# Optimization experiments

Hardware: AMD Instinct MI355X
Metric: run time of the kernel (lower is better)

The kernel has to match this reference:

```python
import jax, jax.numpy as jnp
import numpy as np

K = 2  # top-k experts per token

def setup_inputs() -> dict:
    key = jax.random.key(0)
    ks = jax.random.split(key, 8)
    B, S, D, F, E = 2, 1024, 1024, 4096, 8
    s_in = 1.0 / np.sqrt(D)
    s_mid = 1.0 / np.sqrt(F)
    return {
        "x": jax.random.normal(ks[0], (B, S, D), dtype=jnp.float32),
        "Wr": jax.random.uniform(ks[1], (D, E), jnp.float32, -s_in, s_in),
        "br": jax.random.uniform(ks[2], (E,), jnp.float32, -s_in, s_in),
        "W1": jax.random.uniform(ks[3], (E, D, F), jnp.float32, -s_in, s_in),
        "b1": jax.random.uniform(ks[4], (E, F), jnp.float32, -s_in, s_in),
        "W2": jax.random.uniform(ks[5], (E, F, D), jnp.float32, -s_mid, s_mid),
        "b2": jax.random.uniform(ks[6], (E, D), jnp.float32, -s_mid, s_mid),
    }

def _moe(x, Wr, br, W1, b1, W2, b2):
    E = Wr.shape[1]
    # router (eval mode: no noise)
    logits = jnp.einsum('bsd,de->bse', x, Wr) + br          # [B,S,E]
    topk_logits, topk_idx = jax.lax.top_k(logits, K)        # [B,S,K]
    router_probs = jax.nn.softmax(topk_logits, axis=-1)     # [B,S,K]
    # per-expert combine weight: sum over k slots assigned to expert e
    onehot = jax.nn.one_hot(topk_idx, E, dtype=x.dtype)     # [B,S,K,E]
    w = jnp.einsum('bske,bsk->bse', onehot, router_probs)   # [B,S,E]
    # scan over experts (fixed small E), accumulate weighted expert outputs
    def step(acc, ew):
        W1j, b1j, W2j, b2j, wj = ew                          # wj: [B,S]
        h = jax.nn.gelu(jnp.einsum('bsd,df->bsf', x, W1j) + b1j, approximate=False)
        y = jnp.einsum('bsf,fd->bsd', h, W2j) + b2j
        return acc + y * wj[..., None], None
    out, _ = jax.lax.scan(step, jnp.zeros_like(x),
                          (W1, b1, W2, b2, jnp.transpose(w, (2, 0, 1))))
    return out, router_probs

def reference(x, Wr, br, W1, b1, W2, b2):
    return _moe(x, Wr, br, W1, b1, W2, b2)
```

## Files before the change

kernel.cpp:

```cpp
#include <hip/hip_runtime.h>
#include <hip/hip_bf16.h>
#include <cstdint>

#define TOKENS 2048
#define Dm 1024
#define Fm 4096
#define Em 8

typedef short s16x8 __attribute__((ext_vector_type(8)));
typedef float f32x4 __attribute__((ext_vector_type(4)));

#define GLOAD16(g, l) __builtin_amdgcn_global_load_lds(                     \
    (const __attribute__((address_space(1))) void*)(g),                     \
    (__attribute__((address_space(3))) void*)(l), 16, 0, 0)

__device__ __forceinline__ ushort f2bf(float f) {
  union { float f; uint32_t u; } v; v.f = f;
  uint32_t r = v.u + 0x7fffu + ((v.u >> 16) & 1u);
  return (ushort)(r >> 16);
}

__device__ __forceinline__ void kstep(const ushort* sbuf, int eoff, int aidx,
                                      int bidx, f32x4 (&acc)[4][4]) {
  s16x8 av[4], bv[4];
#pragma unroll
  for (int m = 0; m < 4; ++m)
    av[m] = *(const s16x8*)(sbuf + eoff + aidx + m * 512);
#pragma unroll
  for (int n = 0; n < 4; ++n)
    bv[n] = *(const s16x8*)(sbuf + eoff + 4096 + bidx + n * 512);
#pragma unroll
  for (int m = 0; m < 4; ++m)
#pragma unroll
    for (int n = 0; n < 4; ++n)
      acc[m][n] = __builtin_amdgcn_mfma_f32_16x16x32_bf16(av[m], bv[n], acc[m][n], 0, 0, 0);
}

#define STAGE4(boff) {                                                      \
    char* bb = (char*)sbuf + (boff);                                        \
    GLOAD16(sA0, bb + wid * 1024);                                          \
    GLOAD16(sA1, bb + 4096 + wid * 1024);                                   \
    GLOAD16(sB0, bb + 8192 + wid * 1024);                                   \
    GLOAD16(sB1, bb + 12288 + wid * 1024);                                  \
    sA0 += 32; sA1 += 32; sB0 += 32; sB1 += 32; }

__global__ void transcvt(const float* __restrict__ in, ushort* __restrict__ out,
                         int R, int C) {
  __shared__ float tile[32 * 33];
  int e = blockIdx.z;
  const float* src = in + (size_t)e * R * C;
  ushort* dst = out + (size_t)e * R * C;
  int c0 = blockIdx.x * 32, r0 = blockIdx.y * 32;
  int lr = threadIdx.x >> 5, lc = threadIdx.x & 31;
#pragma unroll
  for (int p = 0; p < 4; ++p)
    tile[(p * 8 + lr) * 33 + lc] = src[(size_t)(r0 + p * 8 + lr) * C + c0 + lc];
  __syncthreads();
#pragma unroll
  for (int p = 0; p < 4; ++p)
    dst[(size_t)(c0 + p * 8 + lr) * R + r0 + lc] = f2bf(tile[lc * 33 + p * 8 + lr]);
}

__global__ void prep(const float* __restrict__ W1, ushort* __restrict__ W1T,
                     const float* __restrict__ W2, ushort* __restrict__ W2T,
                     int do_w2,
                     const float* __restrict__ x, const float* __restrict__ Wr,
                     const float* __restrict__ br, float* __restrict__ probs,
                     int* __restrict__ e_sel, float* __restrict__ w_sel,
                     ushort* __restrict__ xb) {
  __shared__ float shf[32 * 33];
  int b = blockIdx.x;
  if (b < 65536) {
    const float* src;
    ushort* dst;
    size_t sstride, dstride;
    if (b < 32768) {
      int cx = b & 127, ry = (b >> 7) & 31, e = b >> 12;
      src = W1 + ((size_t)e * Dm + ry * 32) * Fm + cx * 32;
      dst = W1T + ((size_t)e * Fm + cx * 32) * Dm + ry * 32;
      sstride = Fm; dstride = Dm;
    } else {
      if (!do_w2) return;
      int b2i = b - 32768;
      int cx = b2i & 31, ry = (b2i >> 5) & 127, e = b2i >> 12;
      src = W2 + ((size_t)e * Fm + ry * 32) * Dm + cx * 32;
      dst = W2T + ((size_t)e * Dm + cx * 32) * Fm + ry * 32;
      sstride = Dm; dstride = Fm;
    }
    int lr = threadIdx.x >> 5, lc = threadIdx.x & 31;
#pragma unroll
    for (int p = 0; p < 4; ++p)
      shf[(p * 8 + lr) * 33 + lc] = src[(size_t)(p * 8 + lr) * sstride + lc];
    __syncthreads();
#pragma unroll
    for (int p = 0; p < 4; ++p)
      dst[(size_t)(p * 8 + lr) * dstride + lc] = f2bf(shf[lc * 33 + p * 8 + lr]);
    return;
  }
  int t = b - 65536;
  const float4* xr4 = (const float4*)(x + (size_t)t * Dm);
  float4 v = xr4[threadIdx.x];
  ushort4 o;
  o.x = f2bf(v.x); o.y = f2bf(v.y); o.z = f2bf(v.z); o.w = f2bf(v.w);
  ((ushort4*)(xb + (size_t)t * Dm))[threadIdx.x] = o;

  int d0 = threadIdx.x * 4;
  const float4* wr4 = (const float4*)(Wr + (size_t)d0 * Em);
  float wv[4][8];
#pragma unroll
  for (int r = 0; r < 4; ++r) {
    float4 a = wr4[r * 2], bq = wr4[r * 2 + 1];
    wv[r][0] = a.x; wv[r][1] = a.y; wv[r][2] = a.z; wv[r][3] = a.w;
    wv[r][4] = bq.x; wv[r][5] = bq.y; wv[r][6] = bq.z; wv[r][7] = bq.w;
  }
  float xs[4] = {v.x, v.y, v.z, v.w};
  float acc[Em];
#pragma unroll
  for (int e = 0; e < Em; ++e)
    acc[e] = xs[0] * wv[0][e] + xs[1] * wv[1][e] + xs[2] * wv[2][e] + xs[3] * wv[3][e];
#pragma unroll
  for (int off = 32; off >= 1; off >>= 1)
#pragma unroll
    for (int e = 0; e < Em; ++e) acc[e] += __shfl_down(acc[e], off);
  float* red = shf;
  int lane = threadIdx.x & 63, wid = threadIdx.x >> 6;
  if (lane == 0)
#pragma unroll
    for (int e = 0; e < Em; ++e) red[wid * 8 + e] = acc[e];
  __syncthreads();
  if (threadIdx.x == 0) {
    float lg[Em];
#pragma unroll
    for (int e = 0; e < Em; ++e)
      lg[e] = red[e] + red[8 + e] + red[16 + e] + red[24 + e] + br[e];
    int i0 = 0;
    for (int e = 1; e < Em; ++e) if (lg[e] > lg[i0]) i0 = e;
    int i1 = -1;
    for (int e = 0; e < Em; ++e) {
      if (e == i0) continue;
      if (i1 < 0 || lg[e] > lg[i1]) i1 = e;
    }
    float d = lg[i1] - lg[i0];
    float tt = expf(d);
    float inv = 1.f / (1.f + tt);
    probs[t * 2] = inv; probs[t * 2 + 1] = tt * inv;
    e_sel[t * 2] = i0; e_sel[t * 2 + 1] = i1;
    w_sel[t * 2] = inv; w_sel[t * 2 + 1] = tt * inv;
  }
}

__global__ void build_lists(const int* __restrict__ e_sel, const float* __restrict__ w_sel,
                            int* __restrict__ tok_of_row, float* __restrict__ w_of_row,
                            int* __restrict__ base, int* __restrict__ npad) {
  __shared__ int cnt[Em], run[Em], sbase[Em];
  __shared__ int wsum[4][Em];
  int tid = threadIdx.x, lane = tid & 63, wid = tid >> 6;
  if (tid < Em) { cnt[tid] = 0; run[tid] = 0; }
  __syncthreads();
  for (int t = tid; t < TOKENS; t += 256) {
    atomicAdd(&cnt[e_sel[2 * t]], 1);
    atomicAdd(&cnt[e_sel[2 * t + 1]], 1);
  }
  __syncthreads();
  if (tid == 0) {
    int b = 0;
    for (int e = 0; e < Em; ++e) {
      base[e] = b; sbase[e] = b;
      int n = cnt[e];
      int p = (n + 127) & ~127;
      npad[e] = p; b += p;
    }
  }
  __syncthreads();
  for (int c = 0; c < TOKENS / 256; ++c) {
    int t = c * 256 + tid;
    int e0 = e_sel[2 * t], e1 = e_sel[2 * t + 1];
    unsigned long long mm[Em];
#pragma unroll
    for (int e = 0; e < Em; ++e) {
      unsigned long long m0 = __ballot(e0 == e);
      unsigned long long m1 = __ballot(e1 == e);
      mm[e] = m0 | m1;
      if (lane == 0) wsum[wid][e] = __popcll(mm[e]);
    }
    __syncthreads();
    unsigned long long below = (1ull << lane) - 1ull;
    {
      int e = e0;
      int p = __popcll(mm[e] & below);
      int pre = 0;
      for (int w = 0; w < wid; ++w) pre += wsum[w][e];
      int row = sbase[e] + run[e] + pre + p;
      tok_of_row[row] = t; w_of_row[row] = w_sel[2 * t];
    }
    {
      int e = e1;
      int p = __popcll(mm[e] & below);
      int pre = 0;
      for (int w = 0; w < wid; ++w) pre += wsum[w][e];
      int row = sbase[e] + run[e] + pre + p;
      tok_of_row[row] = t; w_of_row[row] = w_sel[2 * t + 1];
    }
    __syncthreads();
    if (tid < Em) {
      int s = 0;
      for (int w = 0; w < 4; ++w) s += wsum[w][tid];
      run[tid] += s;
    }
    __syncthreads();
  }
  for (int e = 0; e < Em; ++e) {
    int n = cnt[e];
    int p = (n + 127) & ~127;
    for (int i = n + tid; i < p; i += 256) {
      tok_of_row[sbase[e] + i] = -1;
      w_of_row[sbase[e] + i] = 0.f;
    }
  }
}

__global__ __launch_bounds__(256) void gemm1(
    const ushort* __restrict__ xb, const ushort* __restrict__ W1T,
    const float* __restrict__ b1, ushort* __restrict__ H,
    const int* __restrict__ tok_of_row, const int* __restrict__ base,
    const int* __restrict__ npad) {
  __shared__ ushort sbuf[16384];
  __shared__ int toks[128];
  int tid = threadIdx.x, lane = tid & 63, wid = tid >> 6;
  int e = blockIdx.y >> 4, rt = blockIdx.y & 15;
  int nt = npad[e] >> 7;
  if (rt >= nt) return;
  int row0 = base[e] + rt * 128;
  int n0 = blockIdx.x * 128;
  if (tid < 128) toks[tid] = tok_of_row[row0 + tid];
  __syncthreads();
  int arow = tid >> 2, asub = tid & 3;
  int sw = ((asub ^ ((arow >> 1) & 3)) << 3);
  int t0 = toks[arow];      if (t0 < 0) t0 = 0;
  int t1 = toks[64 + arow]; if (t1 < 0) t1 = 0;
  const ushort* sA0 = xb + (size_t)t0 * Dm + sw;
  const ushort* sA1 = xb + (size_t)t1 * Dm + sw;
  const ushort* sB0 = W1T + ((size_t)e * Fm + n0 + arow) * Dm + sw;
  const ushort* sB1 = sB0 + (size_t)64 * Dm;
  int wr2 = wid >> 1, wc2 = wid & 1;
  int g = lane >> 4, c = (lane >> 1) & 3;
  int aidx = (wr2 * 64 + (lane & 15)) * 32 + ((g ^ c) << 3);
  int bidx = (wc2 * 64 + (lane & 15)) * 32 + ((g ^ c) << 3);
  f32x4 acc[4][4] = {};
  STAGE4(0)
  __syncthreads();
  for (int t = 0; t < 30; t += 2) {
    STAGE4(16384)
    kstep(sbuf, 0, aidx, bidx, acc);
    __syncthreads();
    STAGE4(0)
    kstep(sbuf, 8192, aidx, bidx, acc);
    __syncthreads();
  }
  STAGE4(16384)
  kstep(sbuf, 0, aidx, bidx, acc);
  __syncthreads();
  kstep(sbuf, 8192, aidx, bidx, acc);
#pragma unroll
  for (int p = 0; p < 2; ++p) {
    if (wr2 == p) {
#pragma unroll
      for (int n = 0; n < 4; ++n) {
        int col = wc2 * 64 + (lane & 15) + n * 16;
        float bias = b1[e * Fm + n0 + col];
#pragma unroll
        for (int m = 0; m < 4; ++m) {
#pragma unroll
          for (int j = 0; j < 4; ++j) {
            float v = acc[m][n][j] + bias;
            float gl = 0.5f * v * (1.f + erff(v * 0.70710678118654752f));
            sbuf[(g * 4 + m * 16 + j) * 128 + col] = f2bf(gl);
          }
        }
      }
    }
    __syncthreads();
#pragma unroll
    for (int q = 0; q < 4; ++q) {
      int id = q * 256 + tid;
      int r = id >> 4, ch = id & 15;
      *(s16x8*)(H + (size_t)(row0 + p * 64 + r) * Fm + n0 + ch * 8) =
          *(const s16x8*)(sbuf + r * 128 + ch * 8);
    }
    __syncthreads();
  }
}

__global__ __launch_bounds__(256) void gemm2(
    const ushort* __restrict__ H, const ushort* __restrict__ W2T,
    const float* __restrict__ b2,
    const int* __restrict__ tok_of_row, const float* __restrict__ w_of_row,
    const int* __restrict__ base, const int* __restrict__ npad,
    float* __restrict__ out) {
  __shared__ ushort sbuf[16384];
  __shared__ int toks[128];
  __shared__ float wts[128];
  int tid = threadIdx.x, lane = tid & 63, wid = tid >> 6;
  int e = blockIdx.y >> 4, rt = blockIdx.y & 15;
  int nt = npad[e] >> 7;
  if (rt >= nt) return;
  int row0 = base[e] + rt * 128;
  int n0 = blockIdx.x * 128;
  int k0 = blockIdx.z * (Fm / 2);
  if (tid < 128) {
    toks[tid] = tok_of_row[row0 + tid];
    wts[tid] = w_of_row[row0 + tid];
  }
  __syncthreads();
  int arow = tid >> 2, asub = tid & 3;
  int sw = ((asub ^ ((arow >> 1) & 3)) << 3);
  const ushort* sA0 = H + (size_t)(row0 + arow) * Fm + k0 + sw;
  const ushort* sA1 = sA0 + (size_t)64 * Fm;
  const ushort* sB0 = W2T + ((size_t)e * Dm + n0 + arow) * Fm + k0 + sw;
  const ushort* sB1 = sB0 + (size_t)64 * Fm;
  int wr2 = wid >> 1, wc2 = wid & 1;
  int g = lane >> 4, c = (lane >> 1) & 3;
  int aidx = (wr2 * 64 + (lane & 15)) * 32 + ((g ^ c) << 3);
  int bidx = (wc2 * 64 + (lane & 15)) * 32 + ((g ^ c) << 3);
  f32x4 acc[4][4] = {};
  STAGE4(0)
  __syncthreads();
  for (int t = 0; t < 62; t += 2) {
    STAGE4(16384)
    kstep(sbuf, 0, aidx, bidx, acc);
    __syncthreads();
    STAGE4(0)
    kstep(sbuf, 8192, aidx, bidx, acc);
    __syncthreads();
  }
  STAGE4(16384)
  kstep(sbuf, 0, aidx, bidx, acc);
  __syncthreads();
  kstep(sbuf, 8192, aidx, bidx, acc);
  int rb = wr2 * 64 + g * 4;
  int cb = n0 + wc2 * 64 + (lane & 15);
  int add_bias = (blockIdx.z == 0);
#pragma unroll
  for (int n = 0; n < 4; ++n) {
    int col = cb + n * 16;
    float bias = add_bias ? b2[e * Dm + col] : 0.f;
#pragma unroll
    for (int m = 0; m < 4; ++m) {
      int rl = rb + m * 16;
#pragma unroll
      for (int j = 0; j < 4; ++j) {
        int tok = toks[rl + j];
        if (tok >= 0)
          atomicAdd(&out[(size_t)tok * Dm + col], wts[rl + j] * (acc[m][n][j] + bias));
      }
    }
  }
}

extern "C" void kernel_launch(void* const* d_in, const int* in_sizes, int n_in,
                              void* d_out, int out_size, void* d_ws, size_t ws_size,
                              hipStream_t stream) {
  const float* x  = (const float*)d_in[0];
  const float* Wr = (const float*)d_in[1];
  const float* br = (const float*)d_in[2];
  const float* W1 = (const float*)d_in[3];
  const float* b1 = (const float*)d_in[4];
  const float* W2 = (const float*)d_in[5];
  const float* b2 = (const float*)d_in[6];
  float* out = (float*)d_out;
  float* probs = out + (size_t)TOKENS * Dm;

  char* ws = (char*)d_ws;
  ushort* W1T  = (ushort*)ws;
  ushort* Hbuf = (ushort*)(ws + 67108864);
  ushort* xb   = (ushort*)(ws + 109051904);
  int*   tok_of_row = (int*)(ws + 113246208);
  float* w_of_row   = (float*)(ws + 113266688);
  int*   e_sel      = (int*)(ws + 113287168);
  float* w_sel      = (float*)(ws + 113303552);
  int*   meta       = (int*)(ws + 113319936);
  int sep = (ws_size >= 180429056ULL) ? 1 : 0;
  ushort* W2T = sep ? (ushort*)(ws + 113320192) : W1T;

  hipMemsetAsync(out, 0, (size_t)TOKENS * Dm * sizeof(float), stream);
  prep<<<65536 + TOKENS, 256, 0, stream>>>(W1, W1T, W2, W2T, sep, x, Wr, br,
                                           probs, e_sel, w_sel, xb);
  build_lists<<<1, 256, 0, stream>>>(e_sel, w_sel, tok_of_row, w_of_row,
                                     meta, meta + 8);
  gemm1<<<dim3(32, 128), 256, 0, stream>>>(xb, W1T, b1, Hbuf, tok_of_row,
                                           meta, meta + 8);
  if (!sep)
    transcvt<<<dim3(Dm / 32, Fm / 32, Em), 256, 0, stream>>>(W2, W2T, Fm, Dm);
  gemm2<<<dim3(8, 128, 2), 256, 0, stream>>>(Hbuf, W2T, b2, tok_of_row, w_of_row,
                                             meta, meta + 8, out);
}
```

Measured before the change: 325.9 us.

## Widen weight-transpose tiles, deepen GEMM prefetch pipeline, split gemm2 K four ways

The weight-conversion transpose now handles 64x64 tiles with float4 loads and ushort4 stores, replacing 32x32 scalar accesses and cutting the block count. Both GEMMs now prefetch two stages ahead and use explicit vmcnt/lgkmcnt waits with raw barriers in place of __syncthreads, so global-to-LDS loads can overlap the MFMA work. gemm2 splits K four ways instead of two, which gives more blocks but doubles the atomicAdd traffic into the output. The hand-written waitcnt counts and the LDS reuse after the epilogue must match the load issue order exactly, or the results will be wrong.

Measured after the change: 343.8 us. 5.5% more time.

```diff
diff --git a/kernel.cpp b/kernel.cpp
--- a/kernel.cpp
+++ b/kernel.cpp
@@ -13,6 +13,12 @@
 #define GLOAD16(g, l) __builtin_amdgcn_global_load_lds(                     \
     (const __attribute__((address_space(1))) void*)(g),                     \
     (__attribute__((address_space(3))) void*)(l), 16, 0, 0)
+
+#define VM4 asm volatile("s_waitcnt vmcnt(4)" ::: "memory")
+#define VM0 asm volatile("s_waitcnt vmcnt(0)" ::: "memory")
+#define LG0 asm volatile("s_waitcnt lgkmcnt(0)" ::: "memory")
+#define SCH __builtin_amdgcn_sched_barrier(0)
+#define BAR do { SCH; __builtin_amdgcn_s_barrier(); SCH; } while (0)
 
 __device__ __forceinline__ ushort f2bf(float f) {
   union { float f; uint32_t u; } v; v.f = f;
@@ -68,43 +74,56 @@
                      const float* __restrict__ br, float* __restrict__ probs,
                      int* __restrict__ e_sel, float* __restrict__ w_sel,
                      ushort* __restrict__ xb) {
-  __shared__ float shf[32 * 33];
+  __shared__ float tile[64 * 65];
   int b = blockIdx.x;
-  if (b < 65536) {
+  int tid = threadIdx.x;
+  if (b < 16384) {
     const float* src;
     ushort* dst;
     size_t sstride, dstride;
-    if (b < 32768) {
-      int cx = b & 127, ry = (b >> 7) & 31, e = b >> 12;
-      src = W1 + ((size_t)e * Dm + ry * 32) * Fm + cx * 32;
-      dst = W1T + ((size_t)e * Fm + cx * 32) * Dm + ry * 32;
+    if (b < 8192) {
+      int cx = b & 63, ry = (b >> 6) & 15, e = b >> 10;
+      src = W1 + ((size_t)e * Dm + ry * 64) * Fm + cx * 64;
+      dst = W1T + ((size_t)e * Fm + cx * 64) * Dm + ry * 64;
       sstride = Fm; dstride = Dm;
     } else {
       if (!do_w2) return;
-      int b2i = b - 32768;
-      int cx = b2i & 31, ry = (b2i >> 5) & 127, e = b2i >> 12;
-      src = W2 + ((size_t)e * Fm + ry * 32) * Dm + cx * 32;
-      dst = W2T + ((size_t)e * Dm + cx * 32) * Fm + ry * 32;
+      int j = b - 8192;
+      int cx = j & 15, ry = (j >> 4) & 63, e = j >> 10;
+      src = W2 + ((size_t)e * Fm + ry * 64) * Dm + cx * 64;
+      dst = W2T + ((size_t)e * Dm + cx * 64) * Fm + ry * 64;
       sstride = Dm; dstride = Fm;
     }
-    int lr = threadIdx.x >> 5, lc = threadIdx.x & 31;
-#pragma unroll
-    for (int p = 0; p < 4; ++p)
-      shf[(p * 8 + lr) * 33 + lc] = src[(size_t)(p * 8 + lr) * sstride + lc];
-    __syncthreads();
-#pragma unroll
-    for (int p = 0; p < 4; ++p)
-      dst[(size_t)(p * 8 + lr) * dstride + lc] = f2bf(shf[lc * 33 + p * 8 + lr]);
+    int lr = tid >> 4, lc4 = (tid & 15) * 4;
+#pragma unroll
+    for (int p = 0; p < 4; ++p) {
+      float4 v = *(const float4*)(src + (size_t)(p * 16 + lr) * sstride + lc4);
+      tile[(p * 16 + lr) * 65 + lc4] = v.x;
+      tile[(p * 16 + lr) * 65 + lc4 + 1] = v.y;
+      tile[(p * 16 + lr) * 65 + lc4 + 2] = v.z;
+      tile[(p * 16 + lr) * 65 + lc4 + 3] = v.w;
+    }
+    __syncthreads();
+#pragma unroll
+    for (int p = 0; p < 4; ++p) {
+      int oc = p * 16 + lr;
+      ushort4 o;
+      o.x = f2bf(tile[(lc4 + 0) * 65 + oc]);
+      o.y = f2bf(tile[(lc4 + 1) * 65 + oc]);
+      o.z = f2bf(tile[(lc4 + 2) * 65 + oc]);
+      o.w = f2bf(tile[(lc4 + 3) * 65 + oc]);
+      *(ushort4*)(dst + (size_t)oc * dstride + lc4) = o;
+    }
     return;
   }
-  int t = b - 65536;
+  int t = b - 16384;
   const float4* xr4 = (const float4*)(x + (size_t)t * Dm);
-  float4 v = xr4[threadIdx.x];
+  float4 v = xr4[tid];
   ushort4 o;
   o.x = f2bf(v.x); o.y = f2bf(v.y); o.z = f2bf(v.z); o.w = f2bf(v.w);
-  ((ushort4*)(xb + (size_t)t * Dm))[threadIdx.x] = o;
-
-  int d0 = threadIdx.x * 4;
+  ((ushort4*)(xb + (size_t)t * Dm))[tid] = o;
+
+  int d0 = tid * 4;
   const float4* wr4 = (const float4*)(Wr + (size_t)d0 * Em);
   float wv[4][8];
 #pragma unroll
@@ -122,13 +141,13 @@
   for (int off = 32; off >= 1; off >>= 1)
 #pragma unroll
     for (int e = 0; e < Em; ++e) acc[e] += __shfl_down(acc[e], off);
-  float* red = shf;
-  int lane = threadIdx.x & 63, wid = threadIdx.x >> 6;
+  float* red = tile;
+  int lane = tid & 63, wid = tid >> 6;
   if (lane == 0)
 #pragma unroll
     for (int e = 0; e < Em; ++e) red[wid * 8 + e] = acc[e];
   __syncthreads();
-  if (threadIdx.x == 0) {
+  if (tid == 0) {
     float lg[Em];
 #pragma unroll
     for (int e = 0; e < Em; ++e)
@@ -248,18 +267,20 @@
   int bidx = (wc2 * 64 + (lane & 15)) * 32 + ((g ^ c) << 3);
   f32x4 acc[4][4] = {};
   STAGE4(0)
-  __syncthreads();
+  STAGE4(16384)
   for (int t = 0; t < 30; t += 2) {
+    VM4; BAR;
+    kstep(sbuf, 0, aidx, bidx, acc);
+    LG0; BAR;
+    STAGE4(0)
+    VM4; BAR;
+    kstep(sbuf, 8192, aidx, bidx, acc);
+    LG0; BAR;
     STAGE4(16384)
-    kstep(sbuf, 0, aidx, bidx, acc);
-    __syncthreads();
-    STAGE4(0)
-    kstep(sbuf, 8192, aidx, bidx, acc);
-    __syncthreads();
-  }
-  STAGE4(16384)
+  }
+  VM4; BAR;
   kstep(sbuf, 0, aidx, bidx, acc);
-  __syncthreads();
+  LG0; VM0; BAR;
   kstep(sbuf, 8192, aidx, bidx, acc);
 #pragma unroll
   for (int p = 0; p < 2; ++p) {
@@ -306,7 +327,7 @@
   if (rt >= nt) return;
   int row0 = base[e] + rt * 128;
   int n0 = blockIdx.x * 128;
-  int k0 = blockIdx.z * (Fm / 2);
+  int k0 = blockIdx.z * (Fm / 4);
   if (tid < 128) {
     toks[tid] = tok_of_row[row0 + tid];
     wts[tid] = w_of_row[row0 + tid];
@@ -324,18 +345,20 @@
   int bidx = (wc2 * 64 + (lane & 15)) * 32 + ((g ^ c) << 3);
   f32x4 acc[4][4] = {};
   STAGE4(0)
-  __syncthreads();
-  for (int t = 0; t < 62; t += 2) {
+  STAGE4(16384)
+  for (int t = 0; t < 30; t += 2) {
+    VM4; BAR;
+    kstep(sbuf, 0, aidx, bidx, acc);
+    LG0; BAR;
+    STAGE4(0)
+    VM4; BAR;
+    kstep(sbuf, 8192, aidx, bidx, acc);
+    LG0; BAR;
     STAGE4(16384)
-    kstep(sbuf, 0, aidx, bidx, acc);
-    __syncthreads();
-    STAGE4(0)
-    kstep(sbuf, 8192, aidx, bidx, acc);
-    __syncthreads();
-  }
-  STAGE4(16384)
+  }
+  VM4; BAR;
   kstep(sbuf, 0, aidx, bidx, acc);
-  __syncthreads();
+  LG0; VM0; BAR;
   kstep(sbuf, 8192, aidx, bidx, acc);
   int rb = wr2 * 64 + g * 4;
   int cb = n0 + wc2 * 64 + (lane & 15);
@@ -383,7 +406,7 @@
   ushort* W2T = sep ? (ushort*)(ws + 113320192) : W1T;
 
   hipMemsetAsync(out, 0, (size_t)TOKENS * Dm * sizeof(float), stream);
-  prep<<<65536 + TOKENS, 256, 0, stream>>>(W1, W1T, W2, W2T, sep, x, Wr, br,
+  prep<<<16384 + TOKENS, 256, 0, stream>>>(W1, W1T, W2, W2T, sep, x, Wr, br,
                                            probs, e_sel, w_sel, xb);
   build_lists<<<1, 256, 0, stream>>>(e_sel, w_sel, tok_of_row, w_of_row,
                                      meta, meta + 8);
@@ -391,6 +414,6 @@
                                            meta, meta + 8);
   if (!sep)
     transcvt<<<dim3(Dm / 32, Fm / 32, Em), 256, 0, stream>>>(W2, W2T, Fm, Dm);
-  gemm2<<<dim3(8, 128, 2), 256, 0, stream>>>(Hbuf, W2T, b2, tok_of_row, w_of_row,
+  gemm2<<<dim3(8, 128, 4), 256, 0, stream>>>(Hbuf, W2T, b2, tok_of_row, w_of_row,
                                              meta, meta + 8, out);
 }
```
